# Kernel optimization log

Hardware: AMD Instinct MI355X
Metric: run time of the kernel (lower is better)

Reference implementation:

```python
import jax, jax.numpy as jnp
import numpy as np

B, C, H, W = 8, 256, 64, 64
D = C // 8  # qk proj dim = 32
R = C // 8  # channel-SE reduction dim = 32

def setup_inputs() -> dict:
    key = jax.random.key(0)
    ks = jax.random.split(key, 10)
    s = lambda *sh: 1.0 / np.sqrt(sh[-1])
    return {
        'x':  jax.random.normal(ks[0], (B, C, H, W), jnp.float32),
        'Wq': jax.random.normal(ks[1], (D, C), jnp.float32) * s(D, C),
        'bq': jnp.zeros((D,), jnp.float32),
        'Wk': jax.random.normal(ks[2], (D, C), jnp.float32) * s(D, C),
        'bk': jnp.zeros((D,), jnp.float32),
        'Wv': jax.random.normal(ks[3], (C, C), jnp.float32) * s(C, C),
        'bv': jnp.zeros((C,), jnp.float32),
        'gamma': jnp.ones((1,), jnp.float32),
        'W1': jax.random.normal(ks[4], (R, 2 * C), jnp.float32) * s(R, 2 * C),
        'W2': jax.random.normal(ks[5], (C, R), jnp.float32) * s(C, R),
        'lamb': jnp.ones((1,), jnp.float32),
    }

def reference(x, Wq, bq, Wk, bk, Wv, bv, gamma, W1, W2, lamb):
    b, c, h, w = x.shape
    n = h * w
    xf = x.reshape(b, c, n)  # [B,C,N]
    # --- spatial self-attention (1x1 convs == matmuls over channel dim) ---
    q = jnp.einsum('dc,bcn->bnd', Wq, xf) + bq            # [B,N,D]
    k = jnp.einsum('dc,bcn->bdn', Wk, xf) + bk[:, None]   # [B,D,N]
    attn = jax.nn.softmax(jnp.einsum('bnd,bdm->bnm', q, k), axis=-1)  # [B,N,N]
    v = jnp.einsum('dc,bcn->bdn', Wv, xf) + bv[:, None]   # [B,C,N]
    # out[b,c,m] = sum_n v[b,c,n] * attn[b,m,n]  (torch: bmm(v, attn^T))
    sp = jnp.einsum('bcn,bmn->bcm', v, attn).reshape(b, c, h, w)
    sp = gamma * sp
    # --- channel SE-gate ---
    mean = jnp.mean(xf, axis=-1)                # [B,C]
    std = jnp.std(xf, axis=-1, ddof=1)          # torch.std uses unbiased (ddof=1)
    inp = jnp.concatenate([mean, std], axis=1)  # [B,2C]
    a = jax.nn.sigmoid(jax.nn.relu(inp @ W1.T) @ W2.T)  # [B,C]
    ch = lamb * a[:, :, None, None] * x
    return sp + ch + x
```

## Files before the change

kernel.cpp:

```cpp
#include <hip/hip_runtime.h>
#include <hip/hip_bf16.h>

#define Bb 8
#define Cc 256
#define Nn 4096
#define Dd 32

typedef short bf16x8 __attribute__((ext_vector_type(8)));
typedef short bf16x4 __attribute__((ext_vector_type(4)));
typedef float f32x4 __attribute__((ext_vector_type(4)));
typedef unsigned int u32;

__device__ __forceinline__ void glds16(const void* g, void* l) {
    __builtin_amdgcn_global_load_lds(
        (const __attribute__((address_space(1))) unsigned int*)g,
        (__attribute__((address_space(3))) unsigned int*)l, 16, 0, 0);
}

__device__ __forceinline__ u32 pkbf16(float a, float b) {
    return ((u32)__bfloat16_as_ushort(__float2bfloat16(b)) << 16) |
           (u32)__bfloat16_as_ushort(__float2bfloat16(a));
}

__global__ __launch_bounds__(256) void convt_kernel(
    const float* __restrict__ x, __hip_bfloat16* __restrict__ x_t,
    float* __restrict__ sum_ws, float* __restrict__ sumsq_ws)
{
    __shared__ __hip_bfloat16 tile[64][68];
    const int n0 = blockIdx.x * 64, c0 = blockIdx.y * 64, b = blockIdx.z;
    const int t = threadIdx.x;

#pragma unroll
    for (int i = 0; i < 4; i++) {
        int id = i * 256 + t;
        int row = id >> 4, col4 = id & 15;
        float4 v = *(const float4*)(x + ((size_t)(b * Cc + c0 + row)) * Nn + n0 + col4 * 4);
        bf16x4 bv;
        bv[0] = __bfloat16_as_short(__float2bfloat16(v.x));
        bv[1] = __bfloat16_as_short(__float2bfloat16(v.y));
        bv[2] = __bfloat16_as_short(__float2bfloat16(v.z));
        bv[3] = __bfloat16_as_short(__float2bfloat16(v.w));
        *(bf16x4*)((void*)&tile[row][col4 * 4]) = bv;
        float ls  = v.x + v.y + v.z + v.w;
        float ls2 = v.x * v.x + v.y * v.y + v.z * v.z + v.w * v.w;
        ls  += __shfl_xor(ls, 1, 16);  ls2 += __shfl_xor(ls2, 1, 16);
        ls  += __shfl_xor(ls, 2, 16);  ls2 += __shfl_xor(ls2, 2, 16);
        ls  += __shfl_xor(ls, 4, 16);  ls2 += __shfl_xor(ls2, 4, 16);
        ls  += __shfl_xor(ls, 8, 16);  ls2 += __shfl_xor(ls2, 8, 16);
        if ((t & 15) == 0) {
            atomicAdd(&sum_ws[b * Cc + c0 + row], ls);
            atomicAdd(&sumsq_ws[b * Cc + c0 + row], ls2);
        }
    }
    __syncthreads();
#pragma unroll
    for (int i = 0; i < 2; i++) {
        int id = i * 256 + t;
        int nl = id >> 3, cg = id & 7;
        bf16x8 o;
#pragma unroll
        for (int j = 0; j < 8; j++) o[j] = __bfloat16_as_short(tile[cg * 8 + j][nl]);
        *(bf16x8*)(x_t + ((size_t)(b * Nn + n0 + nl)) * Cc + c0 + cg * 8) = o;
    }
}

__global__ __launch_bounds__(256) void wconv_kernel(
    const float* __restrict__ Wq, const float* __restrict__ Wk, const float* __restrict__ Wv,
    __hip_bfloat16* __restrict__ w_bf)
{
    const int ct = blockIdx.x;
    const int t = threadIdx.x;
#pragma unroll
    for (int i = 0; i < 8; i++) {
        int g = i * 256 + t;
        int row = g >> 5, c8 = g & 31;
        int c0 = c8 * 8;
        int grow = ct * 64 + row;
        const float* src;
        if (grow < 32)       src = Wq + (size_t)grow * Cc + c0;
        else if (grow < 64)  src = Wk + (size_t)(grow - 32) * Cc + c0;
        else                 src = Wv + (size_t)(grow - 64) * Cc + c0;
        float4 v0 = *(const float4*)src;
        float4 v1 = *(const float4*)(src + 4);
        bf16x8 o;
        o[0] = __bfloat16_as_short(__float2bfloat16(v0.x));
        o[1] = __bfloat16_as_short(__float2bfloat16(v0.y));
        o[2] = __bfloat16_as_short(__float2bfloat16(v0.z));
        o[3] = __bfloat16_as_short(__float2bfloat16(v0.w));
        o[4] = __bfloat16_as_short(__float2bfloat16(v1.x));
        o[5] = __bfloat16_as_short(__float2bfloat16(v1.y));
        o[6] = __bfloat16_as_short(__float2bfloat16(v1.z));
        o[7] = __bfloat16_as_short(__float2bfloat16(v1.w));
        int kchunk = c0 >> 5, qd = (c0 & 31) >> 3, cg = row >> 4, rl = row & 15;
        *(bf16x8*)(w_bf + ((size_t)ct * 32 + kchunk * 4 + cg) * 512 + (qd * 16 + rl) * 8) = o;
    }
}

__global__ __launch_bounds__(256, 2) void proj_kernel(
    const __hip_bfloat16* __restrict__ x_t, const __hip_bfloat16* __restrict__ w_bf,
    const float* __restrict__ bq, const float* __restrict__ bk, const float* __restrict__ bv,
    __hip_bfloat16* __restrict__ q_ws, __hip_bfloat16* __restrict__ k_ws,
    __hip_bfloat16* __restrict__ v_ws)
{
    __shared__ __hip_bfloat16 ldsX[32 * 512];
    __shared__ __hip_bfloat16 ldsW[32 * 512];

    const int n0 = blockIdx.x * 64;
    const int b  = blockIdx.y;
    const int t = threadIdx.x;
    const int w = t >> 6, lane = t & 63, quad = lane >> 4, l15 = lane & 15;

#pragma unroll
    for (int j = 0; j < 8; j++) {
        int idx = w * 8 + j;
        int kchunk = idx >> 2, ngrp = idx & 3;
        glds16(x_t + ((size_t)(b * Nn + n0 + ngrp * 16 + l15)) * Cc + kchunk * 32 + quad * 8,
               ldsX + idx * 512);
        glds16(w_bf + (size_t)idx * 512 + lane * 8, ldsW + idx * 512);
    }
    __syncthreads();

    for (int ct = 0; ct < 5; ct++) {
        f32x4 acc[4];
#pragma unroll
        for (int cg = 0; cg < 4; cg++) {
            int gcol = ct * 64 + cg * 16 + l15;
            float bias = (gcol < 32) ? bq[gcol] : (gcol < 64 ? bk[gcol - 32] : bv[gcol - 64]);
            acc[cg] = (f32x4){bias, bias, bias, bias};
        }

#pragma unroll
        for (int kchunk = 0; kchunk < 8; kchunk++) {
            bf16x8 a = *(const bf16x8*)(ldsX + ((kchunk * 4 + w) * 64 + lane) * 8);
#pragma unroll
            for (int cg = 0; cg < 4; cg++) {
                bf16x8 bw = *(const bf16x8*)(ldsW + ((kchunk * 4 + cg) * 64 + lane) * 8);
                acc[cg] = __builtin_amdgcn_mfma_f32_16x16x32_bf16(a, bw, acc[cg], 0, 0, 0);
            }
        }

#pragma unroll
        for (int cg = 0; cg < 4; cg++) {
            int gcol = ct * 64 + cg * 16 + l15;
            int nb = n0 + w * 16 + quad * 4;
            if (gcol < 64) {
                __hip_bfloat16* dst = (gcol < 32) ? q_ws : k_ws;
                int d = gcol & 31;
#pragma unroll
                for (int r = 0; r < 4; r++)
                    dst[((size_t)(b * Nn + nb + r)) * Dd + d] = __float2bfloat16(acc[cg][r]);
            } else {
                int c = gcol - 64;
                bf16x4 o;
#pragma unroll
                for (int r = 0; r < 4; r++) o[r] = __bfloat16_as_short(__float2bfloat16(acc[cg][r]));
                *(bf16x4*)(v_ws + ((size_t)(b * Cc + c)) * Nn + nb) = o;
            }
        }

        if (ct < 4) {
            __syncthreads();
#pragma unroll
            for (int j = 0; j < 8; j++) {
                int idx = w * 8 + j;
                glds16(w_bf + ((size_t)(ct + 1) * 32 + idx) * 512 + lane * 8, ldsW + idx * 512);
            }
            __syncthreads();
        }
    }
}

__global__ __launch_bounds__(256) void gate_kernel(
    const float* __restrict__ sum_ws, const float* __restrict__ sumsq_ws,
    const float* __restrict__ W1, const float* __restrict__ W2,
    const float* __restrict__ lamb, float* __restrict__ coef)
{
    int b = blockIdx.x;
    __shared__ float inp[2 * Cc];
    __shared__ float h[32];
    int t = threadIdx.x;
    float s  = sum_ws[b * Cc + t];
    float s2 = sumsq_ws[b * Cc + t];
    float m   = s / Nn;
    float var = (s2 - (float)Nn * m * m) / (float)(Nn - 1);
    inp[t]      = m;
    inp[Cc + t] = sqrtf(fmaxf(var, 0.f));
    __syncthreads();
    if (t < 32) {
        float a = 0.f;
        for (int i = 0; i < 2 * Cc; i++) a += W1[t * (2 * Cc) + i] * inp[i];
        h[t] = fmaxf(a, 0.f);
    }
    __syncthreads();
    float g = 0.f;
#pragma unroll
    for (int r = 0; r < 32; r++) g += W2[t * 32 + r] * h[r];
    float a = 1.f / (1.f + __expf(-g));
    coef[b * Cc + t] = 1.f + lamb[0] * a;
}

__global__ __launch_bounds__(512, 2) void attn_kernel(
    const __hip_bfloat16* __restrict__ q_ws, const __hip_bfloat16* __restrict__ k_ws,
    const __hip_bfloat16* __restrict__ v_ws, const float* __restrict__ coef,
    const float* __restrict__ x, const float* __restrict__ gamma_p,
    float* __restrict__ out)
{
    extern __shared__ __hip_bfloat16 smem[];
    __hip_bfloat16 *vcur = smem, *vnext = smem + 16384, *vnn = smem + 32768;
    __hip_bfloat16 *kA = smem + 49152, *kB = smem + 53248, *kC = smem + 57344;

    const int b  = blockIdx.x & 7;
    const int m0 = (blockIdx.x >> 3) * 128;
    const int t = threadIdx.x;
    const int w = t >> 6, lane = t & 63, quad = lane >> 4, l15 = lane & 15;
    const int p = w >> 2, pw = w & 3;

    const bf16x8 aq0 = *(const bf16x8*)(q_ws + ((size_t)(b * Nn + m0 + (2 * pw)     * 16 + l15)) * Dd + quad * 8);
    const bf16x8 aq1 = *(const bf16x8*)(q_ws + ((size_t)(b * Nn + m0 + (2 * pw + 1) * 16 + l15)) * Dd + quad * 8);

    const __hip_bfloat16* vsrc[4];
#pragma unroll
    for (int j = 0; j < 4; j++) {
        int idx = w * 4 + j;
        int ch = idx >> 4, tc = idx & 15;
        vsrc[j] = v_ws + ((size_t)(b * Cc + tc * 16 + l15)) * Nn + ch * 32 + quad * 8;
    }
    const int sl15 = (l15 & 3) | ((l15 & 4) << 1) | ((l15 & 8) >> 1);
    const __hip_bfloat16* ksrc = k_ws + ((size_t)(b * Nn + w * 16 + sl15)) * Dd + quad * 8;

#pragma unroll
    for (int j = 0; j < 4; j++) glds16(vsrc[j], vcur + (w * 4 + j) * 512);
#pragma unroll
    for (int j = 0; j < 4; j++) glds16(vsrc[j] + 64, vnext + (w * 4 + j) * 512);
    glds16(ksrc, kA + w * 512);
    glds16(ksrc + (size_t)128 * Dd, kB + w * 512);
    __syncthreads();

    f32x4 acc[2][16];
#pragma unroll
    for (int i = 0; i < 2; i++)
#pragma unroll
        for (int j = 0; j < 16; j++) acc[i][j] = (f32x4){0.f, 0.f, 0.f, 0.f};
    float lsum0 = 0.f, lsum1 = 0.f;

    const int NIT = Nn / 64;

    u32 pc0[2][2], pc1[2][2];
#pragma unroll
    for (int j = 0; j < 2; j++) {
        bf16x8 ak = *(const bf16x8*)(kA + ((2 * p + j) * 64 + lane) * 8);
        f32x4 s0 = __builtin_amdgcn_mfma_f32_16x16x32_bf16(ak, aq0, (f32x4){0.f,0.f,0.f,0.f}, 0, 0, 0);
        f32x4 s1 = __builtin_amdgcn_mfma_f32_16x16x32_bf16(ak, aq1, (f32x4){0.f,0.f,0.f,0.f}, 0, 0, 0);
        float a0 = __expf(s0[0]), a1 = __expf(s0[1]), a2 = __expf(s0[2]), a3 = __expf(s0[3]);
        lsum0 += (a0 + a1) + (a2 + a3);
        pc0[j][0] = pkbf16(a0, a1); pc0[j][1] = pkbf16(a2, a3);
        float b0 = __expf(s1[0]), b1 = __expf(s1[1]), b2 = __expf(s1[2]), b3 = __expf(s1[3]);
        lsum1 += (b0 + b1) + (b2 + b3);
        pc1[j][0] = pkbf16(b0, b1); pc1[j][1] = pkbf16(b2, b3);
    }

    for (int it = 0; it < NIT; it++) {
        if (it + 2 < NIT) {
#pragma unroll
            for (int j = 0; j < 4; j++)
                glds16(vsrc[j] + (size_t)(it + 2) * 64, vnn + (w * 4 + j) * 512);
        }
        if ((it & 1) == 0 && (it >> 1) + 2 < 32)
            glds16(ksrc + (size_t)(((it >> 1) + 2) * 128) * Dd, kC + w * 512);

        auto g0 = __builtin_amdgcn_permlane32_swap(pc0[0][0], pc0[1][0], false, false);
        auto g1 = __builtin_amdgcn_permlane32_swap(pc0[0][1], pc0[1][1], false, false);
        auto h0 = __builtin_amdgcn_permlane32_swap(pc1[0][0], pc1[1][0], false, false);
        auto h1 = __builtin_amdgcn_permlane32_swap(pc1[0][1], pc1[1][1], false, false);
        union { u32 uw[4]; bf16x8 v; } bp0, bp1;
        bp0.uw[0] = g0[0]; bp0.uw[1] = g1[0]; bp0.uw[2] = g0[1]; bp0.uw[3] = g1[1];
        bp1.uw[0] = h0[0]; bp1.uw[1] = h1[0]; bp1.uw[2] = h0[1]; bp1.uw[3] = h1[1];

        u32 pn0[2][2], pn1[2][2];
        const int itn = (it + 1 < NIT) ? it + 1 : NIT - 1;
        const __hip_bfloat16* kb = (((itn >> 1) > (it >> 1)) ? kB : kA) + (itn & 1) * 2048;
        float nls0 = 0.f, nls1 = 0.f;
#pragma unroll
        for (int j = 0; j < 2; j++) {
            bf16x8 ak = *(const bf16x8*)(kb + ((2 * p + j) * 64 + lane) * 8);
            f32x4 s0 = __builtin_amdgcn_mfma_f32_16x16x32_bf16(ak, aq0, (f32x4){0.f,0.f,0.f,0.f}, 0, 0, 0);
            f32x4 s1 = __builtin_amdgcn_mfma_f32_16x16x32_bf16(ak, aq1, (f32x4){0.f,0.f,0.f,0.f}, 0, 0, 0);
            float a0 = __expf(s0[0]), a1 = __expf(s0[1]), a2 = __expf(s0[2]), a3 = __expf(s0[3]);
            nls0 += (a0 + a1) + (a2 + a3);
            pn0[j][0] = pkbf16(a0, a1); pn0[j][1] = pkbf16(a2, a3);
            float b0 = __expf(s1[0]), b1 = __expf(s1[1]), b2 = __expf(s1[2]), b3 = __expf(s1[3]);
            nls1 += (b0 + b1) + (b2 + b3);
            pn1[j][0] = pkbf16(b0, b1); pn1[j][1] = pkbf16(b2, b3);
        }
        if (it + 1 < NIT) { lsum0 += nls0; lsum1 += nls1; }

#pragma unroll
        for (int cf = 0; cf < 16; cf++) {
            bf16x8 av = *(const bf16x8*)(vcur + ((p * 16 + cf) * 64 + lane) * 8);
            acc[0][cf] = __builtin_amdgcn_mfma_f32_16x16x32_bf16(av, bp0.v, acc[0][cf], 0, 0, 0);
            acc[1][cf] = __builtin_amdgcn_mfma_f32_16x16x32_bf16(av, bp1.v, acc[1][cf], 0, 0, 0);
        }

#pragma unroll
        for (int j = 0; j < 2; j++)
#pragma unroll
            for (int k = 0; k < 2; k++) { pc0[j][k] = pn0[j][k]; pc1[j][k] = pn1[j][k]; }

        { __hip_bfloat16* vt = vcur; vcur = vnext; vnext = vnn; vnn = vt; }
        if (it & 1) { __hip_bfloat16* kt = kA; kA = kB; kB = kC; kC = kt; }

        if (it + 2 < NIT)
            asm volatile("s_waitcnt vmcnt(4)\n\ts_barrier" ::: "memory");
        else
            asm volatile("s_waitcnt vmcnt(0)\n\ts_barrier" ::: "memory");
    }

    float* lex = (float*)(smem + 32768);
    lex[w * 128 + lane]      = lsum0;
    lex[w * 128 + 64 + lane] = lsum1;
    f32x4* exv = (f32x4*)smem;
#pragma unroll
    for (int mfi = 0; mfi < 2; mfi++) {
        __syncthreads();
        if (p == 0) {
#pragma unroll
            for (int j = 0; j < 8; j++) exv[(w * 8 + j) * 64 + lane] = acc[mfi][8 + j];
        } else {
#pragma unroll
            for (int j = 0; j < 8; j++) exv[(w * 8 + j) * 64 + lane] = acc[mfi][j];
        }
        __syncthreads();
        if (p == 0) {
#pragma unroll
            for (int j = 0; j < 8; j++) acc[mfi][j] += exv[((w ^ 4) * 8 + j) * 64 + lane];
        } else {
#pragma unroll
            for (int j = 0; j < 8; j++) acc[mfi][8 + j] += exv[((w ^ 4) * 8 + j) * 64 + lane];
        }
        if (mfi == 0) {
            lsum0 += lex[(w ^ 4) * 128 + lane];
            lsum1 += lex[(w ^ 4) * 128 + 64 + lane];
        }
    }

    lsum0 += __shfl_xor(lsum0, 16); lsum0 += __shfl_xor(lsum0, 32);
    lsum1 += __shfl_xor(lsum1, 16); lsum1 += __shfl_xor(lsum1, 32);
    const float g = gamma_p[0];
    const float inv0 = g / lsum0, inv1 = g / lsum1;

    if (p == 0) {
#pragma unroll
        for (int j = 0; j < 8; j++) {
#pragma unroll
            for (int r = 0; r < 4; r++) {
                int c = j * 16 + quad * 4 + r;
                float cfv = coef[b * Cc + c];
                size_t base = ((size_t)(b * Cc + c)) * Nn + m0 + (2 * pw) * 16 + l15;
                out[base]      = acc[0][j][r] * inv0 + cfv * x[base];
                out[base + 16] = acc[1][j][r] * inv1 + cfv * x[base + 16];
            }
        }
    } else {
#pragma unroll
        for (int j = 0; j < 8; j++) {
#pragma unroll
            for (int r = 0; r < 4; r++) {
                int c = (8 + j) * 16 + quad * 4 + r;
                float cfv = coef[b * Cc + c];
                size_t base = ((size_t)(b * Cc + c)) * Nn + m0 + (2 * pw) * 16 + l15;
                out[base]      = acc[0][8 + j][r] * inv0 + cfv * x[base];
                out[base + 16] = acc[1][8 + j][r] * inv1 + cfv * x[base + 16];
            }
        }
    }
}

extern "C" void kernel_launch(void* const* d_in, const int* in_sizes, int n_in,
                              void* d_out, int out_size, void* d_ws, size_t ws_size,
                              hipStream_t stream) {
    const float* x     = (const float*)d_in[0];
    const float* Wq    = (const float*)d_in[1];
    const float* bq    = (const float*)d_in[2];
    const float* Wk    = (const float*)d_in[3];
    const float* bk    = (const float*)d_in[4];
    const float* Wv    = (const float*)d_in[5];
    const float* bv    = (const float*)d_in[6];
    const float* gamma = (const float*)d_in[7];
    const float* W1    = (const float*)d_in[8];
    const float* W2    = (const float*)d_in[9];
    const float* lamb  = (const float*)d_in[10];
    float* out = (float*)d_out;

    char* ws = (char*)d_ws;
    __hip_bfloat16* q_ws = (__hip_bfloat16*)ws;
    __hip_bfloat16* k_ws = (__hip_bfloat16*)(ws + (2u  << 20));
    __hip_bfloat16* v_ws = (__hip_bfloat16*)(ws + (4u  << 20));
    __hip_bfloat16* x_t  = (__hip_bfloat16*)(ws + (20u << 20));
    float* sum_ws   = (float*)(ws + (36u << 20));
    float* sumsq_ws = sum_ws + Bb * Cc;
    float* coef     = sumsq_ws + Bb * Cc;
    __hip_bfloat16* w_bf = (__hip_bfloat16*)(ws + (37u << 20));

    (void)hipFuncSetAttribute((const void*)attn_kernel,
                              hipFuncAttributeMaxDynamicSharedMemorySize, 122880);

    hipMemsetAsync(sum_ws, 0, 2 * Bb * Cc * sizeof(float), stream);
    wconv_kernel<<<5, 256, 0, stream>>>(Wq, Wk, Wv, w_bf);
    convt_kernel<<<dim3(Nn / 64, Cc / 64, Bb), 256, 0, stream>>>(x, x_t, sum_ws, sumsq_ws);
    proj_kernel<<<dim3(Nn / 64, Bb), 256, 0, stream>>>(x_t, w_bf, bq, bk, bv, q_ws, k_ws, v_ws);
    gate_kernel<<<Bb, 256, 0, stream>>>(sum_ws, sumsq_ws, W1, W2, lamb, coef);
    attn_kernel<<<256, 512, 122880, stream>>>(q_ws, k_ws, v_ws, coef, x, gamma, out);
}
```

Baseline: 228.3 us.

## Fuse transpose/stats into projection and SE gate into attention kernel

Removes the standalone convert-transpose kernel by having the projection kernel read fp32 x directly, convert it to bf16, transpose it through an LDS tile into the MFMA operand layout, and accumulate per-channel sum and sum-of-squares. The SE gate MLP is recomputed per block at the start of the attention kernel into shared memory, and the stats-zeroing memset moves into the weight-convert kernel. This cuts two launches and the x_t round trip through global memory. In exchange the projection kernel does serial per-channel-quarter transposes with extra barriers, every attention block redundantly recomputes the gate, and attention launch bounds drop to one block per CU.

```diff
diff --git a/kernel.cpp b/kernel.cpp
--- a/kernel.cpp
+++ b/kernel.cpp
@@ -22,54 +22,13 @@
            (u32)__bfloat16_as_ushort(__float2bfloat16(a));
 }
 
-__global__ __launch_bounds__(256) void convt_kernel(
-    const float* __restrict__ x, __hip_bfloat16* __restrict__ x_t,
-    float* __restrict__ sum_ws, float* __restrict__ sumsq_ws)
-{
-    __shared__ __hip_bfloat16 tile[64][68];
-    const int n0 = blockIdx.x * 64, c0 = blockIdx.y * 64, b = blockIdx.z;
-    const int t = threadIdx.x;
-
-#pragma unroll
-    for (int i = 0; i < 4; i++) {
-        int id = i * 256 + t;
-        int row = id >> 4, col4 = id & 15;
-        float4 v = *(const float4*)(x + ((size_t)(b * Cc + c0 + row)) * Nn + n0 + col4 * 4);
-        bf16x4 bv;
-        bv[0] = __bfloat16_as_short(__float2bfloat16(v.x));
-        bv[1] = __bfloat16_as_short(__float2bfloat16(v.y));
-        bv[2] = __bfloat16_as_short(__float2bfloat16(v.z));
-        bv[3] = __bfloat16_as_short(__float2bfloat16(v.w));
-        *(bf16x4*)((void*)&tile[row][col4 * 4]) = bv;
-        float ls  = v.x + v.y + v.z + v.w;
-        float ls2 = v.x * v.x + v.y * v.y + v.z * v.z + v.w * v.w;
-        ls  += __shfl_xor(ls, 1, 16);  ls2 += __shfl_xor(ls2, 1, 16);
-        ls  += __shfl_xor(ls, 2, 16);  ls2 += __shfl_xor(ls2, 2, 16);
-        ls  += __shfl_xor(ls, 4, 16);  ls2 += __shfl_xor(ls2, 4, 16);
-        ls  += __shfl_xor(ls, 8, 16);  ls2 += __shfl_xor(ls2, 8, 16);
-        if ((t & 15) == 0) {
-            atomicAdd(&sum_ws[b * Cc + c0 + row], ls);
-            atomicAdd(&sumsq_ws[b * Cc + c0 + row], ls2);
-        }
-    }
-    __syncthreads();
-#pragma unroll
-    for (int i = 0; i < 2; i++) {
-        int id = i * 256 + t;
-        int nl = id >> 3, cg = id & 7;
-        bf16x8 o;
-#pragma unroll
-        for (int j = 0; j < 8; j++) o[j] = __bfloat16_as_short(tile[cg * 8 + j][nl]);
-        *(bf16x8*)(x_t + ((size_t)(b * Nn + n0 + nl)) * Cc + c0 + cg * 8) = o;
-    }
-}
-
 __global__ __launch_bounds__(256) void wconv_kernel(
     const float* __restrict__ Wq, const float* __restrict__ Wk, const float* __restrict__ Wv,
-    __hip_bfloat16* __restrict__ w_bf)
+    __hip_bfloat16* __restrict__ w_bf, float* __restrict__ stats )
 {
     const int ct = blockIdx.x;
     const int t = threadIdx.x;
+    for (int k = ct * 256 + t; k < 2 * Bb * Cc; k += 5 * 256) stats[k] = 0.f;
 #pragma unroll
     for (int i = 0; i < 8; i++) {
         int g = i * 256 + t;
@@ -97,11 +56,13 @@
 }
 
 __global__ __launch_bounds__(256, 2) void proj_kernel(
-    const __hip_bfloat16* __restrict__ x_t, const __hip_bfloat16* __restrict__ w_bf,
+    const float* __restrict__ x, const __hip_bfloat16* __restrict__ w_bf,
     const float* __restrict__ bq, const float* __restrict__ bk, const float* __restrict__ bv,
     __hip_bfloat16* __restrict__ q_ws, __hip_bfloat16* __restrict__ k_ws,
-    __hip_bfloat16* __restrict__ v_ws)
+    __hip_bfloat16* __restrict__ v_ws,
+    float* __restrict__ sum_ws, float* __restrict__ sumsq_ws)
 {
+    __shared__ __hip_bfloat16 tile[64][68];
     __shared__ __hip_bfloat16 ldsX[32 * 512];
     __shared__ __hip_bfloat16 ldsW[32 * 512];
 
@@ -113,12 +74,51 @@
 #pragma unroll
     for (int j = 0; j < 8; j++) {
         int idx = w * 8 + j;
-        int kchunk = idx >> 2, ngrp = idx & 3;
-        glds16(x_t + ((size_t)(b * Nn + n0 + ngrp * 16 + l15)) * Cc + kchunk * 32 + quad * 8,
-               ldsX + idx * 512);
         glds16(w_bf + (size_t)idx * 512 + lane * 8, ldsW + idx * 512);
     }
-    __syncthreads();
+
+    for (int cq = 0; cq < 4; cq++) {
+#pragma unroll
+        for (int i = 0; i < 1; i++) {  }
+#pragma unroll
+        for (int i = 0; i < 1; i++) { }
+#pragma unroll
+        for (int i = 0; i < 4; i++) {
+            int id = i * 256 + t;
+            int row = id >> 4, col4 = id & 15;
+            float4 v = *(const float4*)(x + ((size_t)(b * Cc + cq * 64 + row)) * Nn + n0 + col4 * 4);
+            bf16x4 bv4;
+            bv4[0] = __bfloat16_as_short(__float2bfloat16(v.x));
+            bv4[1] = __bfloat16_as_short(__float2bfloat16(v.y));
+            bv4[2] = __bfloat16_as_short(__float2bfloat16(v.z));
+            bv4[3] = __bfloat16_as_short(__float2bfloat16(v.w));
+            *(bf16x4*)((void*)&tile[row][col4 * 4]) = bv4;
+            float ls  = v.x + v.y + v.z + v.w;
+            float ls2 = v.x * v.x + v.y * v.y + v.z * v.z + v.w * v.w;
+            ls  += __shfl_xor(ls, 1, 16);  ls2 += __shfl_xor(ls2, 1, 16);
+            ls  += __shfl_xor(ls, 2, 16);  ls2 += __shfl_xor(ls2, 2, 16);
+            ls  += __shfl_xor(ls, 4, 16);  ls2 += __shfl_xor(ls2, 4, 16);
+            ls  += __shfl_xor(ls, 8, 16);  ls2 += __shfl_xor(ls2, 8, 16);
+            if ((t & 15) == 0) {
+                atomicAdd(&sum_ws[b * Cc + cq * 64 + row], ls);
+                atomicAdd(&sumsq_ws[b * Cc + cq * 64 + row], ls2);
+            }
+        }
+        __syncthreads();
+#pragma unroll
+        for (int it = 0; it < 2; it++) {
+            int id = it * 256 + t;
+            int nl = id >> 3, cg = id & 7;
+            bf16x8 o;
+#pragma unroll
+            for (int j = 0; j < 8; j++) o[j] = __bfloat16_as_short(tile[cg * 8 + j][nl]);
+            int kchunk = cq * 2 + (cg >> 2);
+            int cquad  = cg & 3;
+            int ngrp = nl >> 4, nlo = nl & 15;
+            *(bf16x8*)(ldsX + ((size_t)(kchunk * 4 + ngrp) * 512) + (cquad * 16 + nlo) * 8) = o;
+        }
+        __syncthreads();
+    }
 
     for (int ct = 0; ct < 5; ct++) {
         f32x4 acc[4];
@@ -170,50 +170,56 @@
     }
 }
 
-__global__ __launch_bounds__(256) void gate_kernel(
+__global__ __launch_bounds__(512, 1) void attn_kernel(
+    const __hip_bfloat16* __restrict__ q_ws, const __hip_bfloat16* __restrict__ k_ws,
+    const __hip_bfloat16* __restrict__ v_ws,
     const float* __restrict__ sum_ws, const float* __restrict__ sumsq_ws,
     const float* __restrict__ W1, const float* __restrict__ W2,
-    const float* __restrict__ lamb, float* __restrict__ coef)
-{
-    int b = blockIdx.x;
-    __shared__ float inp[2 * Cc];
-    __shared__ float h[32];
-    int t = threadIdx.x;
-    float s  = sum_ws[b * Cc + t];
-    float s2 = sumsq_ws[b * Cc + t];
-    float m   = s / Nn;
-    float var = (s2 - (float)Nn * m * m) / (float)(Nn - 1);
-    inp[t]      = m;
-    inp[Cc + t] = sqrtf(fmaxf(var, 0.f));
-    __syncthreads();
-    if (t < 32) {
-        float a = 0.f;
-        for (int i = 0; i < 2 * Cc; i++) a += W1[t * (2 * Cc) + i] * inp[i];
-        h[t] = fmaxf(a, 0.f);
-    }
-    __syncthreads();
-    float g = 0.f;
-#pragma unroll
-    for (int r = 0; r < 32; r++) g += W2[t * 32 + r] * h[r];
-    float a = 1.f / (1.f + __expf(-g));
-    coef[b * Cc + t] = 1.f + lamb[0] * a;
-}
-
-__global__ __launch_bounds__(512, 2) void attn_kernel(
-    const __hip_bfloat16* __restrict__ q_ws, const __hip_bfloat16* __restrict__ k_ws,
-    const __hip_bfloat16* __restrict__ v_ws, const float* __restrict__ coef,
+    const float* __restrict__ lamb_p,
     const float* __restrict__ x, const float* __restrict__ gamma_p,
     float* __restrict__ out)
 {
     extern __shared__ __hip_bfloat16 smem[];
     __hip_bfloat16 *vcur = smem, *vnext = smem + 16384, *vnn = smem + 32768;
     __hip_bfloat16 *kA = smem + 49152, *kB = smem + 53248, *kC = smem + 57344;
+    float* coef_s = (float*)((char*)smem + 122880);
 
     const int b  = blockIdx.x & 7;
     const int m0 = (blockIdx.x >> 3) * 128;
     const int t = threadIdx.x;
     const int w = t >> 6, lane = t & 63, quad = lane >> 4, l15 = lane & 15;
     const int p = w >> 2, pw = w & 3;
+
+    {
+        float* inp_s = (float*)smem;
+        float* h_s   = (float*)smem + 512;
+        if (t < 256) {
+            float s  = sum_ws[b * Cc + t];
+            float s2 = sumsq_ws[b * Cc + t];
+            float m   = s / Nn;
+            float var = (s2 - (float)Nn * m * m) / (float)(Nn - 1);
+            inp_s[t]       = m;
+            inp_s[256 + t] = sqrtf(fmaxf(var, 0.f));
+        }
+        __syncthreads();
+        {
+            int r = t >> 4, s5 = t & 15;
+            float a = 0.f;
+#pragma unroll
+            for (int i = 0; i < 32; i++) a += W1[r * 512 + s5 * 32 + i] * inp_s[s5 * 32 + i];
+            a += __shfl_xor(a, 1, 16); a += __shfl_xor(a, 2, 16);
+            a += __shfl_xor(a, 4, 16); a += __shfl_xor(a, 8, 16);
+            if (s5 == 0) h_s[r] = fmaxf(a, 0.f);
+        }
+        __syncthreads();
+        if (t < 256) {
+            float gg = 0.f;
+#pragma unroll
+            for (int r = 0; r < 32; r++) gg += W2[t * 32 + r] * h_s[r];
+            coef_s[t] = 1.f + lamb_p[0] * (1.f / (1.f + __expf(-gg)));
+        }
+        __syncthreads();
+    }
 
     const bf16x8 aq0 = *(const bf16x8*)(q_ws + ((size_t)(b * Nn + m0 + (2 * pw)     * 16 + l15)) * Dd + quad * 8);
     const bf16x8 aq1 = *(const bf16x8*)(q_ws + ((size_t)(b * Nn + m0 + (2 * pw + 1) * 16 + l15)) * Dd + quad * 8);
@@ -354,7 +360,7 @@
 #pragma unroll
             for (int r = 0; r < 4; r++) {
                 int c = j * 16 + quad * 4 + r;
-                float cfv = coef[b * Cc + c];
+                float cfv = coef_s[c];
                 size_t base = ((size_t)(b * Cc + c)) * Nn + m0 + (2 * pw) * 16 + l15;
                 out[base]      = acc[0][j][r] * inv0 + cfv * x[base];
                 out[base + 16] = acc[1][j][r] * inv1 + cfv * x[base + 16];
@@ -366,7 +372,7 @@
 #pragma unroll
             for (int r = 0; r < 4; r++) {
                 int c = (8 + j) * 16 + quad * 4 + r;
-                float cfv = coef[b * Cc + c];
+                float cfv = coef_s[c];
                 size_t base = ((size_t)(b * Cc + c)) * Nn + m0 + (2 * pw) * 16 + l15;
                 out[base]      = acc[0][8 + j][r] * inv0 + cfv * x[base];
                 out[base + 16] = acc[1][8 + j][r] * inv1 + cfv * x[base + 16];
@@ -395,19 +401,16 @@
     __hip_bfloat16* q_ws = (__hip_bfloat16*)ws;
     __hip_bfloat16* k_ws = (__hip_bfloat16*)(ws + (2u  << 20));
     __hip_bfloat16* v_ws = (__hip_bfloat16*)(ws + (4u  << 20));
-    __hip_bfloat16* x_t  = (__hip_bfloat16*)(ws + (20u << 20));
     float* sum_ws   = (float*)(ws + (36u << 20));
     float* sumsq_ws = sum_ws + Bb * Cc;
-    float* coef     = sumsq_ws + Bb * Cc;
     __hip_bfloat16* w_bf = (__hip_bfloat16*)(ws + (37u << 20));
 
     (void)hipFuncSetAttribute((const void*)attn_kernel,
-                              hipFuncAttributeMaxDynamicSharedMemorySize, 122880);
-
-    hipMemsetAsync(sum_ws, 0, 2 * Bb * Cc * sizeof(float), stream);
-    wconv_kernel<<<5, 256, 0, stream>>>(Wq, Wk, Wv, w_bf);
-    convt_kernel<<<dim3(Nn / 64, Cc / 64, Bb), 256, 0, stream>>>(x, x_t, sum_ws, sumsq_ws);
-    proj_kernel<<<dim3(Nn / 64, Bb), 256, 0, stream>>>(x_t, w_bf, bq, bk, bv, q_ws, k_ws, v_ws);
-    gate_kernel<<<Bb, 256, 0, stream>>>(sum_ws, sumsq_ws, W1, W2, lamb, coef);
-    attn_kernel<<<256, 512, 122880, stream>>>(q_ws, k_ws, v_ws, coef, x, gamma, out);
-}
+                              hipFuncAttributeMaxDynamicSharedMemorySize, 123904);
+
+    wconv_kernel<<<5, 256, 0, stream>>>(Wq, Wk, Wv, w_bf, sum_ws);
+    proj_kernel<<<dim3(Nn / 64, Bb), 256, 0, stream>>>(x, w_bf, bq, bk, bv,
+                                                       q_ws, k_ws, v_ws, sum_ws, sumsq_ws);
+    attn_kernel<<<256, 512, 123904, stream>>>(q_ws, k_ws, v_ws, sum_ws, sumsq_ws,
+                                              W1, W2, lamb, x, gamma, out);
+}
```

New measurement: 221.5 us. 3.0% less time.
